# Performance work log

Hardware: AMD Instinct MI355X
Metric: run time of the kernel (lower is better)

Reference implementation:

```python
import jax, jax.numpy as jnp
import numpy as np

NH, HD, NKV = 32, 128, 8      # query heads, head dim, kv heads (GQA group = 4)
BS = 16                        # cache block size
NB = 4096                      # number of cache blocks
MB = 128                       # max blocks per sequence (max kv len = 2048)
S = 32                         # decode sequences, 1 new token each
SCALE = 1.0 / float(np.sqrt(HD))
F8 = jnp.float8_e4m3fn


def setup_inputs() -> dict:
    key = jax.random.key(0)
    ks = jax.random.split(key, 10)
    q = jax.random.normal(ks[0], (S, NH * HD), dtype=jnp.float32)
    k = jax.random.normal(ks[1], (S, NKV * HD), dtype=jnp.float32)
    v = jax.random.normal(ks[2], (S, NKV * HD), dtype=jnp.float32)
    k_cache = jax.random.normal(ks[3], (NB, BS, NKV, HD), dtype=jnp.float32)
    v_cache = jax.random.normal(ks[4], (NB, BS, NKV, HD), dtype=jnp.float32)
    k_scale = jax.random.uniform(ks[5], (NKV,), minval=0.5, maxval=1.5, dtype=jnp.float32)
    v_scale = jax.random.uniform(ks[6], (NKV,), minval=0.5, maxval=1.5, dtype=jnp.float32)
    # unique blocks per sequence: permutation of all NB blocks (NB == S*MB)
    block_tables = jax.random.permutation(ks[7], NB).reshape(S, MB).astype(jnp.int64)
    context_lens = jax.random.randint(ks[8], (S,), 64, MB * BS + 1).astype(jnp.int64)
    # slot of the newly generated token: position context_len-1 inside its block table
    last = context_lens - 1
    blk = jnp.take_along_axis(block_tables, (last // BS)[:, None], axis=1)[:, 0]
    slot_mapping = (blk * BS + last % BS).astype(jnp.int64)
    return {"q": q, "k": k, "v": v, "k_cache": k_cache, "v_cache": v_cache,
            "k_scale": k_scale, "v_scale": v_scale, "slot_mapping": slot_mapping,
            "block_tables": block_tables, "context_lens": context_lens}


def reference(q, k, v, k_cache, v_cache, k_scale, v_scale, slot_mapping, block_tables, context_lens):
    s = q.shape[0]
    G = NH // NKV
    qr = q.reshape(s, NKV, G, HD)              # [S, nkvh, g, hd]
    kn = k.reshape(s, NKV, HD)                 # [S, nkvh, hd]
    vn = v.reshape(s, NKV, HD)
    # --- store_kvcache: quantize new K/V to fp8 with per-kv-head scale, scatter at slot_mapping
    kq = (kn / k_scale[None, :, None]).astype(F8).astype(jnp.float32)
    vq = (vn / v_scale[None, :, None]).astype(F8).astype(jnp.float32)
    kc = k_cache.reshape(NB * BS, NKV, HD).at[slot_mapping].set(kq)
    vc = v_cache.reshape(NB * BS, NKV, HD).at[slot_mapping].set(vq)
    # --- FP8 dequant of cache (view-as-fp8, * scale, -> bf16), as in unified 'static' decode
    kd = (kc.astype(F8).astype(jnp.float32) * k_scale[None, :, None]).astype(jnp.bfloat16)
    vd = (vc.astype(F8).astype(jnp.float32) * v_scale[None, :, None]).astype(jnp.bfloat16)
    # --- paged gather via block tables -> per-seq contiguous KV of length L = MB*BS
    slots = (block_tables[:, :, None] * BS + jnp.arange(BS)[None, None, :]).reshape(s, MB * BS)
    Kg = kd[slots]                              # [S, L, nkvh, hd]
    Vg = vd[slots]
    L = MB * BS
    ctx = jnp.maximum(context_lens, 1)
    # --- GQA decode attention (1 query token per sequence)
    scores = jnp.einsum('shgd,slhd->shgl', qr.astype(jnp.float32), Kg.astype(jnp.float32)) * SCALE
    mask = jnp.arange(L)[None, :] < ctx[:, None]            # [S, L]
    scores = jnp.where(mask[:, None, None, :], scores, -jnp.inf)
    p = jax.nn.softmax(scores, axis=-1)
    o = jnp.einsum('shgl,slhd->shgd', p, Vg.astype(jnp.float32))
    return o.reshape(s, NH * HD)
```

## Files before the change

kernel.cpp:

```cpp
#include <hip/hip_runtime.h>
#include <hip/hip_bf16.h>

#define NH   32
#define HD   128
#define NKV  8
#define GQ   4
#define BS   16
#define NB   4096
#define MB   128
#define SEQ  32
#define WPG  8
#define UPW  8
#define NSPLIT (WPG*UPW)
#define UNROLL 4

__constant__ float SCALE_RSQRT = 0.08838834764831845f;

typedef float v2f __attribute__((ext_vector_type(2)));

__device__ __forceinline__ float bf16r(float x) {
  unsigned u = __float_as_uint(x);
  u = (u + 0x7fffu + ((u >> 16) & 1u)) & 0xffff0000u;
  return __uint_as_float(u);
}

__device__ __forceinline__ float4 deq4(float4 x, float sc) {
  int p0 = __builtin_amdgcn_cvt_pk_fp8_f32(x.x, x.y, 0, false);
  int p1 = __builtin_amdgcn_cvt_pk_fp8_f32(x.z, x.w, 0, false);
  v2f a = __builtin_amdgcn_cvt_pk_f32_fp8(p0, false);
  v2f b = __builtin_amdgcn_cvt_pk_f32_fp8(p1, false);
  float4 r;
  r.x = bf16r(a.x * sc);
  r.y = bf16r(a.y * sc);
  r.z = bf16r(b.x * sc);
  r.w = bf16r(b.y * sc);
  return r;
}

__global__ __launch_bounds__(256, 4)
void attn_split(const float* __restrict__ q,
                const float* __restrict__ knew,
                const float* __restrict__ vnew,
                const float* __restrict__ k_cache,
                const float* __restrict__ v_cache,
                const float* __restrict__ k_scale,
                const float* __restrict__ v_scale,
                const int* __restrict__ block_tables,
                const int* __restrict__ context_lens,
                float* __restrict__ o_part,
                float2* __restrict__ ml_part) {
  const int wg = blockIdx.x;
  const int wgsub = wg % WPG;
  const int h = (wg / WPG) % NKV;
  const int s = wg / (WPG * NKV);
  const int tid = threadIdx.x;
  const int lane = tid & 31;
  const int unit = tid >> 5;
  const int ug = wgsub * UPW + unit;
  const int dbase = lane * 4;

  __shared__ int bt[MB];
  __shared__ float so[UPW][GQ][HD];
  __shared__ float2 sml[UPW][GQ];

  if (tid < MB) bt[tid] = block_tables[s * MB + tid];
  __syncthreads();

  const int ctx = context_lens[s];
  const int last = ctx - 1;
  const float ks = k_scale[h];
  const float vs = v_scale[h];

  float4 qv[GQ];
#pragma unroll
  for (int g = 0; g < GQ; ++g) {
    float4 t = *(const float4*)(q + ((size_t)s * NH + h * GQ + g) * HD + dbase);
    qv[g].x = t.x * SCALE_RSQRT;
    qv[g].y = t.y * SCALE_RSQRT;
    qv[g].z = t.z * SCALE_RSQRT;
    qv[g].w = t.w * SCALE_RSQRT;
  }

  float m[GQ], l[GQ];
  float4 oacc[GQ];
#pragma unroll
  for (int g = 0; g < GQ; ++g) {
    m[g] = -1e30f;
    l[g] = 0.0f;
    oacc[g] = make_float4(0.f, 0.f, 0.f, 0.f);
  }

  if (ug == (last & (NSPLIT - 1))) {
    float4 kk = *(const float4*)(knew + ((size_t)s * NKV + h) * HD + dbase);
    float4 vt = *(const float4*)(vnew + ((size_t)s * NKV + h) * HD + dbase);
    kk.x /= ks; kk.y /= ks; kk.z /= ks; kk.w /= ks;
    vt.x /= vs; vt.y /= vs; vt.z /= vs; vt.w /= vs;
    kk = deq4(kk, ks);
    vt = deq4(vt, vs);
#pragma unroll
    for (int g = 0; g < GQ; ++g) {
      float d = kk.x * qv[g].x + kk.y * qv[g].y + kk.z * qv[g].z + kk.w * qv[g].w;
      d += __shfl_xor(d, 1);
      d += __shfl_xor(d, 2);
      d += __shfl_xor(d, 4);
      d += __shfl_xor(d, 8);
      d += __shfl_xor(d, 16);
      m[g] = d;
      l[g] = 1.0f;
      oacc[g] = vt;
    }
  }

  for (int t0 = ug; t0 < ctx; t0 += NSPLIT * UNROLL) {
    float4 kk[UNROLL], vv[UNROLL];
    bool val[UNROLL];
#pragma unroll
    for (int i = 0; i < UNROLL; ++i) {
      int t = t0 + i * NSPLIT;
      val[i] = (t < ctx) && (t != last);
      kk[i] = make_float4(0.f, 0.f, 0.f, 0.f);
      vv[i] = make_float4(0.f, 0.f, 0.f, 0.f);
      if (val[i]) {
        int blk = bt[t >> 4];
        size_t off = (((size_t)blk * BS + (t & (BS - 1))) * NKV + h) * HD + dbase;
        kk[i] = *(const float4*)(k_cache + off);
        vv[i] = *(const float4*)(v_cache + off);
      }
    }

    float sc[UNROLL][GQ];
#pragma unroll
    for (int i = 0; i < UNROLL; ++i) {
      float4 kd = deq4(kk[i], ks);
      vv[i] = deq4(vv[i], vs);
#pragma unroll
      for (int g = 0; g < GQ; ++g) {
        float d = kd.x * qv[g].x + kd.y * qv[g].y + kd.z * qv[g].z + kd.w * qv[g].w;
        d += __shfl_xor(d, 1);
        d += __shfl_xor(d, 2);
        d += __shfl_xor(d, 4);
        d += __shfl_xor(d, 8);
        d += __shfl_xor(d, 16);
        sc[i][g] = val[i] ? d : -1e30f;
      }
    }

#pragma unroll
    for (int g = 0; g < GQ; ++g) {
      float tm = sc[0][g];
#pragma unroll
      for (int i = 1; i < UNROLL; ++i) tm = fmaxf(tm, sc[i][g]);
      float mnew = fmaxf(m[g], tm);
      float alpha = __expf(m[g] - mnew);
      float p[UNROLL];
      float lad = 0.f;
#pragma unroll
      for (int i = 0; i < UNROLL; ++i) {
        p[i] = __expf(sc[i][g] - mnew);
        lad += p[i];
      }
      l[g] = l[g] * alpha + lad;
      float4 acc = make_float4(0.f, 0.f, 0.f, 0.f);
#pragma unroll
      for (int i = 0; i < UNROLL; ++i) {
        acc.x += p[i] * vv[i].x;
        acc.y += p[i] * vv[i].y;
        acc.z += p[i] * vv[i].z;
        acc.w += p[i] * vv[i].w;
      }
      oacc[g].x = oacc[g].x * alpha + acc.x;
      oacc[g].y = oacc[g].y * alpha + acc.y;
      oacc[g].z = oacc[g].z * alpha + acc.z;
      oacc[g].w = oacc[g].w * alpha + acc.w;
      m[g] = mnew;
    }
  }

#pragma unroll
  for (int g = 0; g < GQ; ++g)
    *(float4*)&so[unit][g][dbase] = oacc[g];
  if (lane == 0) {
#pragma unroll
    for (int g = 0; g < GQ; ++g) sml[unit][g] = make_float2(m[g], l[g]);
  }
  __syncthreads();

  if (tid < 128) {
    int g = tid >> 5;
    int ln = tid & 31;
    float M = -1e30f;
#pragma unroll
    for (int u = 0; u < UPW; ++u) M = fmaxf(M, sml[u][g].x);
    float L = 0.f;
    float4 acc = make_float4(0.f, 0.f, 0.f, 0.f);
#pragma unroll
    for (int u = 0; u < UPW; ++u) {
      float w = __expf(sml[u][g].x - M);
      L += sml[u][g].y * w;
      float4 t = *(const float4*)&so[u][g][ln * 4];
      acc.x += w * t.x;
      acc.y += w * t.y;
      acc.z += w * t.z;
      acc.w += w * t.w;
    }
    size_t ob = ((((size_t)s * NKV + h) * WPG + wgsub) * GQ + g) * HD + ln * 4;
    *(float4*)(o_part + ob) = acc;
    if (ln == 0)
      ml_part[(((size_t)s * NKV + h) * WPG + wgsub) * GQ + g] = make_float2(M, L);
  }
}

__global__ void combine_splits(const float* __restrict__ o_part,
                               const float2* __restrict__ ml_part,
                               float* __restrict__ out) {
  int b = blockIdx.x;
  int h = b % NKV;
  int s = b / NKV;
  int d = threadIdx.x;
#pragma unroll
  for (int g = 0; g < GQ; ++g) {
    float2 ml[WPG];
    float M = -1e30f;
#pragma unroll
    for (int i = 0; i < WPG; ++i) {
      ml[i] = ml_part[(((size_t)s * NKV + h) * WPG + i) * GQ + g];
      M = fmaxf(M, ml[i].x);
    }
    float L = 0.f;
    float acc = 0.f;
#pragma unroll
    for (int i = 0; i < WPG; ++i) {
      float w = __expf(ml[i].x - M);
      L += ml[i].y * w;
      acc += w * o_part[((((size_t)s * NKV + h) * WPG + i) * GQ + g) * HD + d];
    }
    out[((size_t)s * NH + h * GQ + g) * HD + d] = acc / L;
  }
}

extern "C" void kernel_launch(void* const* d_in, const int* in_sizes, int n_in,
                              void* d_out, int out_size, void* d_ws, size_t ws_size,
                              hipStream_t stream) {
  const float* q        = (const float*)d_in[0];
  const float* k        = (const float*)d_in[1];
  const float* v        = (const float*)d_in[2];
  const float* k_cache  = (const float*)d_in[3];
  const float* v_cache  = (const float*)d_in[4];
  const float* k_scale  = (const float*)d_in[5];
  const float* v_scale  = (const float*)d_in[6];
  const int*   btables  = (const int*)d_in[8];
  const int*   ctx_lens = (const int*)d_in[9];
  float*       out      = (float*)d_out;

  float*  o_part  = (float*)d_ws;
  float2* ml_part = (float2*)((char*)d_ws +
                     (size_t)SEQ * NKV * WPG * GQ * HD * sizeof(float));

  attn_split<<<SEQ * NKV * WPG, 256, 0, stream>>>(
      q, k, v, k_cache, v_cache, k_scale, v_scale, btables, ctx_lens,
      o_part, ml_part);

  combine_splits<<<SEQ * NKV, 128, 0, stream>>>(o_part, ml_part, out);
}
```

Before: 486.5 us.

## Double-buffer KV loads through LDS with async global_load_lds

Replaces direct register loads of K/V cache rows with asynchronous global_load_lds transfers into double-buffered LDS tiles, so the next tile is fetched while the current one is dequantized and accumulated. The tile depth per iteration drops from 4 tokens to 2, and the last-token handling moves into the loop bound rather than a per-token check. The output staging buffer now reuses the K LDS region. This adds explicit vmcnt waits and relies on the lane layout of 64-wide waves (two 32-lane units per wave), which is fragile. The clamped token index keeps out-of-range loads in bounds at the cost of some redundant traffic.

```diff
diff --git a/kernel.cpp b/kernel.cpp
--- a/kernel.cpp
+++ b/kernel.cpp
@@ -12,7 +12,14 @@
 #define WPG  8
 #define UPW  8
 #define NSPLIT (WPG*UPW)
-#define UNROLL 4
+#define TI   2
+#define NBUF 2
+
+#define WAIT_VM4 0x0F74
+#define WAIT_VM0 0x0F70
+
+#define AS1 __attribute__((address_space(1)))
+#define AS3 __attribute__((address_space(3)))
 
 __constant__ float SCALE_RSQRT = 0.08838834764831845f;
 
@@ -56,11 +63,14 @@
   const int tid = threadIdx.x;
   const int lane = tid & 31;
   const int unit = tid >> 5;
+  const int wave = tid >> 6;
+  const int uw = unit & 1;
   const int ug = wgsub * UPW + unit;
   const int dbase = lane * 4;
 
   __shared__ int bt[MB];
-  __shared__ float so[UPW][GQ][HD];
+  __shared__ __align__(16) float ldsK[NBUF][4][TI][256];
+  __shared__ __align__(16) float ldsV[NBUF][4][TI][256];
   __shared__ float2 sml[UPW][GQ];
 
   if (tid < MB) bt[tid] = block_tables[s * MB + tid];
@@ -90,7 +100,9 @@
     oacc[g] = make_float4(0.f, 0.f, 0.f, 0.f);
   }
 
-  if (ug == (last & (NSPLIT - 1))) {
+  const bool owns_last = (ug == (last & (NSPLIT - 1)));
+
+  if (owns_last) {
     float4 kk = *(const float4*)(knew + ((size_t)s * NKV + h) * HD + dbase);
     float4 vt = *(const float4*)(vnew + ((size_t)s * NKV + h) * HD + dbase);
     kk.x /= ks; kk.y /= ks; kk.z /= ks; kk.w /= ks;
@@ -111,71 +123,83 @@
     }
   }
 
-  for (int t0 = ug; t0 < ctx; t0 += NSPLIT * UNROLL) {
-    float4 kk[UNROLL], vv[UNROLL];
-    bool val[UNROLL];
-#pragma unroll
-    for (int i = 0; i < UNROLL; ++i) {
-      int t = t0 + i * NSPLIT;
-      val[i] = (t < ctx) && (t != last);
-      kk[i] = make_float4(0.f, 0.f, 0.f, 0.f);
-      vv[i] = make_float4(0.f, 0.f, 0.f, 0.f);
-      if (val[i]) {
-        int blk = bt[t >> 4];
-        size_t off = (((size_t)blk * BS + (t & (BS - 1))) * NKV + h) * HD + dbase;
-        kk[i] = *(const float4*)(k_cache + off);
-        vv[i] = *(const float4*)(v_cache + off);
-      }
-    }
-
-    float sc[UNROLL][GQ];
-#pragma unroll
-    for (int i = 0; i < UNROLL; ++i) {
-      float4 kd = deq4(kk[i], ks);
-      vv[i] = deq4(vv[i], vs);
+  const int tend = owns_last ? last : ctx;
+  const int n = (tend > ug) ? ((tend - ug + NSPLIT - 1) >> 6) : 0;
+  const int tmax = max(tend - 1, ug);
+
+  const int ug_o = ug ^ 1;
+  const int tend_o = (ug_o == (last & (NSPLIT - 1))) ? last : ctx;
+  const int n_o = (tend_o > ug_o) ? ((tend_o - ug_o + NSPLIT - 1) >> 6) : 0;
+  const int nw = max(n, n_o);
+  const int ntile = (nw + TI - 1) / TI;
+
+#define STAGE(JB, B)                                                          \
+  do {                                                                        \
+    _Pragma("unroll") for (int i_ = 0; i_ < TI; ++i_) {                       \
+      int t_ = ug + ((JB) + i_) * NSPLIT;                                     \
+      t_ = min(t_, tmax);                                                     \
+      int blk_ = bt[t_ >> 4];                                                 \
+      size_t off_ = (((size_t)blk_ * BS + (t_ & (BS - 1))) * NKV + h) * HD +  \
+                    dbase;                                                    \
+      __builtin_amdgcn_global_load_lds(                                       \
+          (const AS1 void*)(k_cache + off_),                                  \
+          (AS3 void*)&ldsK[B][wave][i_][0], 16, 0, 0);                        \
+      __builtin_amdgcn_global_load_lds(                                       \
+          (const AS1 void*)(v_cache + off_),                                  \
+          (AS3 void*)&ldsV[B][wave][i_][0], 16, 0, 0);                        \
+    }                                                                         \
+  } while (0)
+
+  if (ntile > 0) STAGE(0, 0);
+
+  for (int j = 0, b = 0; j < ntile; ++j, b ^= 1) {
+    if (j + 1 < ntile) {
+      STAGE((j + 1) * TI, b ^ 1);
+      __builtin_amdgcn_s_waitcnt(WAIT_VM4);
+    } else {
+      __builtin_amdgcn_s_waitcnt(WAIT_VM0);
+    }
+
+    float sc_[TI][GQ];
+    float4 vd_[TI];
+#pragma unroll
+    for (int i = 0; i < TI; ++i) {
+      float4 kk = *(const float4*)&ldsK[b][wave][i][uw * 128 + dbase];
+      float4 vv = *(const float4*)&ldsV[b][wave][i][uw * 128 + dbase];
+      float4 kd = deq4(kk, ks);
+      vd_[i] = deq4(vv, vs);
+      int t = ug + (j * TI + i) * NSPLIT;
+      bool valid = (t < tend);
 #pragma unroll
       for (int g = 0; g < GQ; ++g) {
-        float d = kd.x * qv[g].x + kd.y * qv[g].y + kd.z * qv[g].z + kd.w * qv[g].w;
+        float d = kd.x * qv[g].x + kd.y * qv[g].y + kd.z * qv[g].z +
+                  kd.w * qv[g].w;
         d += __shfl_xor(d, 1);
         d += __shfl_xor(d, 2);
         d += __shfl_xor(d, 4);
         d += __shfl_xor(d, 8);
         d += __shfl_xor(d, 16);
-        sc[i][g] = val[i] ? d : -1e30f;
+        sc_[i][g] = valid ? d : -1e30f;
       }
     }
-
 #pragma unroll
     for (int g = 0; g < GQ; ++g) {
-      float tm = sc[0][g];
-#pragma unroll
-      for (int i = 1; i < UNROLL; ++i) tm = fmaxf(tm, sc[i][g]);
+      float tm = fmaxf(sc_[0][g], sc_[1][g]);
       float mnew = fmaxf(m[g], tm);
       float alpha = __expf(m[g] - mnew);
-      float p[UNROLL];
-      float lad = 0.f;
-#pragma unroll
-      for (int i = 0; i < UNROLL; ++i) {
-        p[i] = __expf(sc[i][g] - mnew);
-        lad += p[i];
-      }
-      l[g] = l[g] * alpha + lad;
-      float4 acc = make_float4(0.f, 0.f, 0.f, 0.f);
-#pragma unroll
-      for (int i = 0; i < UNROLL; ++i) {
-        acc.x += p[i] * vv[i].x;
-        acc.y += p[i] * vv[i].y;
-        acc.z += p[i] * vv[i].z;
-        acc.w += p[i] * vv[i].w;
-      }
-      oacc[g].x = oacc[g].x * alpha + acc.x;
-      oacc[g].y = oacc[g].y * alpha + acc.y;
-      oacc[g].z = oacc[g].z * alpha + acc.z;
-      oacc[g].w = oacc[g].w * alpha + acc.w;
+      float p0 = __expf(sc_[0][g] - mnew);
+      float p1 = __expf(sc_[1][g] - mnew);
+      l[g] = l[g] * alpha + (p0 + p1);
+      oacc[g].x = oacc[g].x * alpha + p0 * vd_[0].x + p1 * vd_[1].x;
+      oacc[g].y = oacc[g].y * alpha + p0 * vd_[0].y + p1 * vd_[1].y;
+      oacc[g].z = oacc[g].z * alpha + p0 * vd_[0].z + p1 * vd_[1].z;
+      oacc[g].w = oacc[g].w * alpha + p0 * vd_[0].w + p1 * vd_[1].w;
       m[g] = mnew;
     }
   }
 
+  __syncthreads();
+  float (*so)[GQ][HD] = (float (*)[GQ][HD])ldsK;
 #pragma unroll
   for (int g = 0; g < GQ; ++g)
     *(float4*)&so[unit][g][dbase] = oacc[g];
```

Measured after the change: 488.5 us. No clear change (+0.4%).
